# Performance work log

Measured on AMD Instinct MI355X. Metric: run time of the kernel, lower is better.

Reference implementation:

```python
import jax, jax.numpy as jnp
import numpy as np

EPS = 1e-5
B, CIN, COUT, H, W = 32, 512, 512, 56, 56
K = 4            # kernel_num
A = 32           # attention_channel = max(int(512*0.0625), 16)


def setup_inputs() -> dict:
    key = jax.random.key(0)
    ks = jax.random.split(key, 16)
    s = lambda fan: 1.0 / np.sqrt(fan)
    return {
        "x": jax.random.normal(ks[0], (B, CIN, H, W), jnp.float32),
        # attention trunk: global-avgpool -> fc -> bn -> relu
        "fc_w": jax.random.normal(ks[1], (A, CIN), jnp.float32) * s(CIN),
        "abn_g": jnp.ones((A,), jnp.float32),
        "abn_b": jnp.zeros((A,), jnp.float32),
        "abn_m": jax.random.normal(ks[2], (A,), jnp.float32) * 0.1,
        "abn_v": jax.random.uniform(ks[3], (A,), jnp.float32, 0.5, 1.5),
        # channel / filter / kernel attention heads
        "ch_w": jax.random.normal(ks[4], (CIN, A), jnp.float32) * s(A),
        "ch_b": jnp.zeros((CIN,), jnp.float32),
        "fl_w": jax.random.normal(ks[5], (COUT, A), jnp.float32) * s(A),
        "fl_b": jnp.zeros((COUT,), jnp.float32),
        "kn_w": jax.random.normal(ks[6], (K, A), jnp.float32) * s(A),
        "kn_b": jnp.zeros((K,), jnp.float32),
        # base 1x1 conv weight bank [kernel_num, out, in] (1x1 spatial squeezed)
        "weight": jax.random.normal(ks[7], (K, COUT, CIN), jnp.float32) * s(CIN),
        # output BatchNorm2d (eval mode: running stats)
        "bn_g": jnp.ones((COUT,), jnp.float32),
        "bn_b": jnp.zeros((COUT,), jnp.float32),
        "bn_m": jax.random.normal(ks[8], (COUT,), jnp.float32) * 0.1,
        "bn_v": jax.random.uniform(ks[9], (COUT,), jnp.float32, 0.5, 1.5),
    }


def reference(x, fc_w, abn_g, abn_b, abn_m, abn_v,
              ch_w, ch_b, fl_w, fl_b, kn_w, kn_b,
              weight, bn_g, bn_b, bn_m, bn_v):
    # ---- omni-dimensional attention (kernel_size=1 => spatial attn skipped) ----
    pooled = jnp.mean(x, axis=(2, 3))                       # [B, Cin]
    h = pooled @ fc_w.T                                     # [B, A]
    h = (h - abn_m) * (abn_g / jnp.sqrt(abn_v + EPS)) + abn_b
    h = jax.nn.relu(h)
    ch_att = jax.nn.sigmoid(h @ ch_w.T + ch_b)              # [B, Cin]
    fl_att = jax.nn.sigmoid(h @ fl_w.T + fl_b)              # [B, Cout]
    kn_att = jax.nn.softmax(h @ kn_w.T + kn_b, axis=1)      # [B, K] (temperature=1)
    # ---- per-sample aggregated 1x1 kernel + grouped(batch) pointwise conv ----
    agg_w = jnp.einsum('bk,koc->boc', kn_att, weight)       # [B, Cout, Cin]
    xm = x * ch_att[:, :, None, None]                       # channel attention
    y = jnp.einsum('bchw,boc->bohw', xm, agg_w)             # batched 1x1 conv
    y = y * fl_att[:, :, None, None]                        # filter attention
    # ---- BatchNorm2d (inference) ----
    inv = bn_g / jnp.sqrt(bn_v + EPS)
    y = (y - bn_m[None, :, None, None]) * inv[None, :, None, None] + bn_b[None, :, None, None]
    return y
```

## Files before the change

### kernel.cpp

```cpp
#include <hip/hip_runtime.h>
#include <math.h>

#define BATCH 32
#define CIN   512
#define COUT  512
#define HW    3136
#define KNUM  4
#define ADIM  32
#define EPS   1e-5f

static constexpr size_t XT_OFF    = 0;
static constexpr size_t WF_OFF    = 102760448;
static constexpr size_t PART_OFF  = 119537664;
static constexpr size_t CH_OFF    = 122748928;
static constexpr size_t FLINV_OFF = 122814464;
static constexpr size_t KN_OFF    = 122880000;

typedef __attribute__((ext_vector_type(8))) short short8;
typedef __attribute__((ext_vector_type(4))) float float4v;

typedef const unsigned int __attribute__((address_space(1)))* gas_ptr;
typedef unsigned int __attribute__((address_space(3)))* lds_ptr;

#define WAITVM(N) asm volatile("s_waitcnt vmcnt(" #N ")" ::: "memory")
#define BARRIER() do { __builtin_amdgcn_s_barrier(); asm volatile("" ::: "memory"); } while (0)

__device__ __forceinline__ unsigned short f2bf(float f) {
  unsigned int u = __float_as_uint(f);
  u += 0x7FFFu + ((u >> 16) & 1u);
  return (unsigned short)(u >> 16);
}

__global__ __launch_bounds__(256) void transpose_pool(
    const float* __restrict__ x, unsigned short* __restrict__ xT,
    float* __restrict__ part) {
  __shared__ unsigned short T[64 * 128];
  const int pb = blockIdx.x * 64;
  const int cb = blockIdx.y * 128;
  const int b  = blockIdx.z;
  const int t  = threadIdx.x;
  const int pq = t & 15;
  const int ch = t >> 4;

  float s[4][2];
  #pragma unroll
  for (int it = 0; it < 4; ++it) {
    const int cp = it * 16 + ch;
    const int c  = cb + cp * 2;
    const float* xp = x + (size_t)(b * CIN + c) * HW + pb + pq * 4;
    float4 v0 = *(const float4*)(xp);
    float4 v1 = *(const float4*)(xp + HW);
    s[it][0] = v0.x + v0.y + v0.z + v0.w;
    s[it][1] = v1.x + v1.y + v1.z + v1.w;
    const int dbase = (((cp >> 2) ^ pq) & 15) * 4 + (cp & 3);
    const float* f0 = (const float*)&v0;
    const float* f1 = (const float*)&v1;
    #pragma unroll
    for (int j = 0; j < 4; ++j) {
      const int p = pq * 4 + j;
      unsigned int w = (unsigned int)f2bf(f0[j]) |
                       ((unsigned int)f2bf(f1[j]) << 16);
      *(unsigned int*)&T[p * 128 + dbase * 2] = w;
    }
  }
  #pragma unroll
  for (int it = 0; it < 4; ++it) {
    #pragma unroll
    for (int e = 0; e < 2; ++e) {
      float v = s[it][e];
      #pragma unroll
      for (int off = 8; off > 0; off >>= 1) v += __shfl_down(v, off, 16);
      if (pq == 0)
        part[((size_t)b * 49 + blockIdx.x) * 512 + cb + (it * 16 + ch) * 2 + e] = v;
    }
  }
  __syncthreads();
  const int cg = t & 15;
  const int rb = t >> 4;
  #pragma unroll
  for (int itr = 0; itr < 4; ++itr) {
    const int p = rb + itr * 16;
    const int key = (p >> 2) & 15;
    uint4 r = *(const uint4*)&T[p * 128 + ((cg ^ key) & 15) * 8];
    *(uint4*)(xT + (size_t)(b * HW + pb + p) * CIN + cb + cg * 8) = r;
  }
}

__global__ __launch_bounds__(256) void attn_all(
    const float* __restrict__ part, const float* __restrict__ fc_w,
    const float* __restrict__ abn_g, const float* __restrict__ abn_b,
    const float* __restrict__ abn_m, const float* __restrict__ abn_v,
    const float* __restrict__ kn_w, const float* __restrict__ kn_b,
    const float* __restrict__ ch_w, const float* __restrict__ ch_b,
    const float* __restrict__ fl_w, const float* __restrict__ fl_b,
    const float* __restrict__ bn_g, const float* __restrict__ bn_v,
    float* __restrict__ ch_out, float* __restrict__ flinv_out,
    float* __restrict__ kn_out) {
  __shared__ float pooledS[CIN];
  __shared__ float hs[ADIM];
  const int b = blockIdx.x, t = threadIdx.x;
  #pragma unroll
  for (int idx = t; idx < CIN; idx += 256) {
    float s = 0.f;
    for (int j = 0; j < 49; ++j) s += part[((size_t)b * 49 + j) * 512 + idx];
    pooledS[idx] = s;
  }
  __syncthreads();
  {
    const int a = t >> 3, pz = t & 7;
    const float* fr = fc_w + a * CIN + pz * 64;
    const float* pp = pooledS + pz * 64;
    float s = 0.f;
    #pragma unroll 8
    for (int c = 0; c < 64; ++c) s += pp[c] * fr[c];
    #pragma unroll
    for (int off = 4; off > 0; off >>= 1) s += __shfl_down(s, off, 8);
    if (pz == 0) {
      s *= (1.0f / (float)HW);
      float vv = (s - abn_m[a]) * (abn_g[a] * rsqrtf(abn_v[a] + EPS)) + abn_b[a];
      hs[a] = fmaxf(vv, 0.f);
    }
  }
  __syncthreads();
  if (t == 0) {
    float lg[KNUM]; float mx = -1e30f;
    for (int k = 0; k < KNUM; ++k) {
      float acc = kn_b[k];
      for (int aa = 0; aa < ADIM; ++aa) acc += hs[aa] * kn_w[k * ADIM + aa];
      lg[k] = acc; mx = fmaxf(mx, acc);
    }
    float ssum = 0.f;
    for (int k = 0; k < KNUM; ++k) { lg[k] = expf(lg[k] - mx); ssum += lg[k]; }
    for (int k = 0; k < KNUM; ++k) kn_out[b * KNUM + k] = lg[k] / ssum;
  }
  #pragma unroll
  for (int c = t; c < CIN; c += 256) {
    const float* wr = ch_w + c * ADIM;
    float acc = ch_b[c];
    #pragma unroll
    for (int aa = 0; aa < ADIM; ++aa) acc += hs[aa] * wr[aa];
    ch_out[b * CIN + c] = 1.f / (1.f + expf(-acc));
  }
  #pragma unroll
  for (int o = t; o < COUT; o += 256) {
    const float* wr = fl_w + o * ADIM;
    float acc = fl_b[o];
    #pragma unroll
    for (int aa = 0; aa < ADIM; ++aa) acc += hs[aa] * wr[aa];
    float sig = 1.f / (1.f + expf(-acc));
    flinv_out[b * COUT + o] = sig * (bn_g[o] * rsqrtf(bn_v[o] + EPS));
  }
}

__global__ __launch_bounds__(256) void build_wf(
    const float* __restrict__ weight, const float* __restrict__ kn,
    const float* __restrict__ ch, const float* __restrict__ flinv,
    unsigned short* __restrict__ Wf) {
  const int och = blockIdx.x, b = blockIdx.y, t = threadIdx.x;
  const int o0 = och * 16;
  const float k0 = kn[b * KNUM + 0], k1 = kn[b * KNUM + 1];
  const float k2 = kn[b * KNUM + 2], k3 = kn[b * KNUM + 3];
  #pragma unroll
  for (int i = 0; i < 8; ++i) {
    int cell = i * 1024 + t * 4;
    int ol = cell >> 9, c = cell & 511;
    int o = o0 + ol;
    float fi = flinv[b * COUT + o];
    const float* wp = weight + (size_t)o * CIN + c;
    float4 w0 = *(const float4*)(wp);
    float4 w1 = *(const float4*)(wp + 1 * CIN * COUT);
    float4 w2 = *(const float4*)(wp + 2 * CIN * COUT);
    float4 w3 = *(const float4*)(wp + 3 * CIN * COUT);
    float4 cv = *(const float4*)(ch + b * CIN + c);
    ushort4 r;
    r.x = f2bf((k0 * w0.x + k1 * w1.x + k2 * w2.x + k3 * w3.x) * cv.x * fi);
    r.y = f2bf((k0 * w0.y + k1 * w1.y + k2 * w2.y + k3 * w3.y) * cv.y * fi);
    r.z = f2bf((k0 * w0.z + k1 * w1.z + k2 * w2.z + k3 * w3.z) * cv.z * fi);
    r.w = f2bf((k0 * w0.w + k1 * w1.w + k2 * w2.w + k3 * w3.w) * cv.w * fi);
    *(ushort4*)(Wf + (size_t)(b * COUT + o) * CIN + c) = r;
  }
}

__global__ __launch_bounds__(512, 2) void gemm_kernel(
    const unsigned short* __restrict__ xT, const unsigned short* __restrict__ Wf,
    const float* __restrict__ bn_g, const float* __restrict__ bn_b,
    const float* __restrict__ bn_m, const float* __restrict__ bn_v,
    float* __restrict__ y) {
  extern __shared__ unsigned short L[];
  const int id = blockIdx.x;
  const int wg = (id & 7) * 104 + (id >> 3);
  const int ot = wg & 1;
  const int rem = wg >> 1;
  const int pt = rem % 13;
  const int b  = rem / 13;
  const int o0 = ot * 256, p0 = pt * 256;
  const int t = threadIdx.x;
  const int wave = t >> 6, lane = t & 63;
  const int wm = wave >> 2, wn = wave & 3;

  const unsigned short* Ab = Wf + (size_t)b * COUT * CIN;
  const unsigned short* Bb = xT + (size_t)b * HW * CIN;

  const int rr = lane >> 2;
  const int gp = (lane & 3) ^ ((lane >> 3) & 3);
  const unsigned short* aS[2];
  const unsigned short* bS[2];
  int dOff[2];
  #pragma unroll
  for (int q = 0; q < 2; ++q) {
    const int m = q * 8 + wave;
    dOff[q] = m * 512;
    aS[q] = Ab + (size_t)(o0 + m * 16 + rr) * CIN + gp * 8;
    int brow = p0 + m * 16 + rr;
    if (brow > HW - 1) brow = HW - 1;
    bS[q] = Bb + (size_t)brow * CIN + gp * 8;
  }

  float4v acc[8][4];
  #pragma unroll
  for (int i = 0; i < 8; ++i)
    #pragma unroll
    for (int j = 0; j < 4; ++j)
      #pragma unroll
      for (int r = 0; r < 4; ++r) acc[i][j][r] = 0.f;

  const int arow = lane & 15;
  const int kgrp = lane >> 4;
  const int sl = (kgrp ^ ((arow >> 1) & 3)) * 8;

  auto stage = [&](int tt) {
    const int bufb = (tt & 3) * 16384;
    const int co = tt * 32;
    #pragma unroll
    for (int q = 0; q < 2; ++q)
      __builtin_amdgcn_global_load_lds((gas_ptr)(const void*)(aS[q] + co),
          (lds_ptr)(void*)&L[bufb + dOff[q]], 16, 0, 0);
    #pragma unroll
    for (int q = 0; q < 2; ++q)
      __builtin_amdgcn_global_load_lds((gas_ptr)(const void*)(bS[q] + co),
          (lds_ptr)(void*)&L[bufb + 8192 + dOff[q]], 16, 0, 0);
  };

  auto compute = [&](int tt) {
    const int bufb = (tt & 3) * 16384;
    short8 af[8], bv[4];
    #pragma unroll
    for (int i = 0; i < 8; ++i)
      af[i] = *(const short8*)&L[bufb + (wm * 128 + i * 16 + arow) * 32 + sl];
    #pragma unroll
    for (int j = 0; j < 4; ++j)
      bv[j] = *(const short8*)&L[bufb + 8192 + (wn * 64 + j * 16 + arow) * 32 + sl];
    __builtin_amdgcn_s_setprio(1);
    #pragma unroll
    for (int i = 0; i < 8; ++i)
      #pragma unroll
      for (int j = 0; j < 4; ++j)
        acc[i][j] = __builtin_amdgcn_mfma_f32_16x16x32_bf16(af[i], bv[j], acc[i][j], 0, 0, 0);
    __builtin_amdgcn_s_setprio(0);
  };

  stage(0); stage(1); stage(2);
  WAITVM(8);
  BARRIER();
  #pragma unroll 1
  for (int tt = 0; tt < 13; ++tt) {
    stage(tt + 3);
    compute(tt);
    WAITVM(8);
    BARRIER();
  }
  compute(13); WAITVM(4); BARRIER();
  compute(14); WAITVM(0); BARRIER();
  compute(15);

  const int rowq = (lane >> 4) * 4;
  const int coln = lane & 15;
  #pragma unroll
  for (int i = 0; i < 8; ++i) {
    const int obase = o0 + wm * 128 + i * 16 + rowq;
    float bet[4];
    #pragma unroll
    for (int r = 0; r < 4; ++r) {
      const int o = obase + r;
      const float inv = bn_g[o] * rsqrtf(bn_v[o] + EPS);
      bet[r] = bn_b[o] - bn_m[o] * inv;
    }
    #pragma unroll
    for (int j = 0; j < 4; ++j) {
      const int p = p0 + wn * 64 + j * 16 + coln;
      if (p < HW) {
        #pragma unroll
        for (int r = 0; r < 4; ++r)
          y[(size_t)(b * COUT + obase + r) * HW + p] = acc[i][j][r] + bet[r];
      }
    }
  }
}

extern "C" void kernel_launch(void* const* d_in, const int* in_sizes, int n_in,
                              void* d_out, int out_size, void* d_ws, size_t ws_size,
                              hipStream_t stream) {
  (void)in_sizes; (void)n_in; (void)out_size; (void)ws_size;
  const float* x     = (const float*)d_in[0];
  const float* fc_w  = (const float*)d_in[1];
  const float* abn_g = (const float*)d_in[2];
  const float* abn_b = (const float*)d_in[3];
  const float* abn_m = (const float*)d_in[4];
  const float* abn_v = (const float*)d_in[5];
  const float* ch_w  = (const float*)d_in[6];
  const float* ch_b  = (const float*)d_in[7];
  const float* fl_w  = (const float*)d_in[8];
  const float* fl_b  = (const float*)d_in[9];
  const float* kn_w  = (const float*)d_in[10];
  const float* kn_b  = (const float*)d_in[11];
  const float* weight= (const float*)d_in[12];
  const float* bn_g  = (const float*)d_in[13];
  const float* bn_b  = (const float*)d_in[14];
  const float* bn_m  = (const float*)d_in[15];
  const float* bn_v  = (const float*)d_in[16];
  float* out = (float*)d_out;

  char* ws = (char*)d_ws;
  unsigned short* xT = (unsigned short*)(ws + XT_OFF);
  unsigned short* Wf = (unsigned short*)(ws + WF_OFF);
  float* part  = (float*)(ws + PART_OFF);
  float* ch    = (float*)(ws + CH_OFF);
  float* flinv = (float*)(ws + FLINV_OFF);
  float* kn    = (float*)(ws + KN_OFF);

  static bool attr_done = false;
  if (!attr_done) {
    hipFuncSetAttribute((const void*)gemm_kernel,
                        hipFuncAttributeMaxDynamicSharedMemorySize, 131072);
    attr_done = true;
  }

  transpose_pool<<<dim3(49, 4, BATCH), 256, 0, stream>>>(x, xT, part);
  attn_all<<<BATCH, 256, 0, stream>>>(part, fc_w, abn_g, abn_b, abn_m, abn_v,
                                      kn_w, kn_b, ch_w, ch_b, fl_w, fl_b,
                                      bn_g, bn_v, ch, flinv, kn);
  build_wf<<<dim3(32, BATCH), 256, 0, stream>>>(weight, kn, ch, flinv, Wf);
  gemm_kernel<<<dim3(832), dim3(512), 131072, stream>>>(xT, Wf, bn_g, bn_b, bn_m, bn_v, out);
}
```

Baseline: 485.4 us.

## Shrink GEMM tile to 128x128 with double-buffered 4-wave blocks

Replaces the 256x256-tile, 8-wave, 4-stage-pipelined GEMM with a 128x128 tile using 4 waves and a two-buffer LDS pipeline with static shared memory. The grid becomes a plain 3D launch without the XCD-aware block remapping, and the priority hints and dynamic-LDS attribute setup are removed. The intent is more resident blocks per CU and finer-grained scheduling. The cost is halved operand reuse per tile, a shallower prefetch depth and an extra barrier per k-step.

```diff
diff --git a/kernel.cpp b/kernel.cpp
--- a/kernel.cpp
+++ b/kernel.cpp
@@ -23,7 +23,7 @@
 typedef unsigned int __attribute__((address_space(3)))* lds_ptr;
 
 #define WAITVM(N) asm volatile("s_waitcnt vmcnt(" #N ")" ::: "memory")
-#define BARRIER() do { __builtin_amdgcn_s_barrier(); asm volatile("" ::: "memory"); } while (0)
+#define WAITLGKM0() asm volatile("s_waitcnt lgkmcnt(0)" ::: "memory")
 
 __device__ __forceinline__ unsigned short f2bf(float f) {
   unsigned int u = __float_as_uint(f);
@@ -181,22 +181,17 @@
   }
 }
 
-__global__ __launch_bounds__(512, 2) void gemm_kernel(
+__global__ __launch_bounds__(256, 4) void gemm_kernel(
     const unsigned short* __restrict__ xT, const unsigned short* __restrict__ Wf,
     const float* __restrict__ bn_g, const float* __restrict__ bn_b,
     const float* __restrict__ bn_m, const float* __restrict__ bn_v,
     float* __restrict__ y) {
-  extern __shared__ unsigned short L[];
-  const int id = blockIdx.x;
-  const int wg = (id & 7) * 104 + (id >> 3);
-  const int ot = wg & 1;
-  const int rem = wg >> 1;
-  const int pt = rem % 13;
-  const int b  = rem / 13;
-  const int o0 = ot * 256, p0 = pt * 256;
+  __shared__ unsigned short L[2 * 8192];
+  const int ot = blockIdx.x, pt = blockIdx.y, b = blockIdx.z;
+  const int o0 = ot * 128, p0 = pt * 128;
   const int t = threadIdx.x;
   const int wave = t >> 6, lane = t & 63;
-  const int wm = wave >> 2, wn = wave & 3;
+  const int wm = wave & 1, wn = wave >> 1;
 
   const unsigned short* Ab = Wf + (size_t)b * COUT * CIN;
   const unsigned short* Bb = xT + (size_t)b * HW * CIN;
@@ -208,7 +203,7 @@
   int dOff[2];
   #pragma unroll
   for (int q = 0; q < 2; ++q) {
-    const int m = q * 8 + wave;
+    const int m = q * 4 + wave;
     dOff[q] = m * 512;
     aS[q] = Ab + (size_t)(o0 + m * 16 + rr) * CIN + gp * 8;
     int brow = p0 + m * 16 + rr;
@@ -216,9 +211,9 @@
     bS[q] = Bb + (size_t)brow * CIN + gp * 8;
   }
 
-  float4v acc[8][4];
-  #pragma unroll
-  for (int i = 0; i < 8; ++i)
+  float4v acc[4][4];
+  #pragma unroll
+  for (int i = 0; i < 4; ++i)
     #pragma unroll
     for (int j = 0; j < 4; ++j)
       #pragma unroll
@@ -229,7 +224,7 @@
   const int sl = (kgrp ^ ((arow >> 1) & 3)) * 8;
 
   auto stage = [&](int tt) {
-    const int bufb = (tt & 3) * 16384;
+    const int bufb = (tt & 1) * 8192;
     const int co = tt * 32;
     #pragma unroll
     for (int q = 0; q < 2; ++q)
@@ -238,46 +233,44 @@
     #pragma unroll
     for (int q = 0; q < 2; ++q)
       __builtin_amdgcn_global_load_lds((gas_ptr)(const void*)(bS[q] + co),
-          (lds_ptr)(void*)&L[bufb + 8192 + dOff[q]], 16, 0, 0);
+          (lds_ptr)(void*)&L[bufb + 4096 + dOff[q]], 16, 0, 0);
   };
 
   auto compute = [&](int tt) {
-    const int bufb = (tt & 3) * 16384;
-    short8 af[8], bv[4];
-    #pragma unroll
-    for (int i = 0; i < 8; ++i)
-      af[i] = *(const short8*)&L[bufb + (wm * 128 + i * 16 + arow) * 32 + sl];
+    const int bufb = (tt & 1) * 8192;
+    short8 af[4], bv[4];
+    #pragma unroll
+    for (int i = 0; i < 4; ++i)
+      af[i] = *(const short8*)&L[bufb + (wm * 64 + i * 16 + arow) * 32 + sl];
     #pragma unroll
     for (int j = 0; j < 4; ++j)
-      bv[j] = *(const short8*)&L[bufb + 8192 + (wn * 64 + j * 16 + arow) * 32 + sl];
-    __builtin_amdgcn_s_setprio(1);
-    #pragma unroll
-    for (int i = 0; i < 8; ++i)
+      bv[j] = *(const short8*)&L[bufb + 4096 + (wn * 64 + j * 16 + arow) * 32 + sl];
+    #pragma unroll
+    for (int i = 0; i < 4; ++i)
       #pragma unroll
       for (int j = 0; j < 4; ++j)
         acc[i][j] = __builtin_amdgcn_mfma_f32_16x16x32_bf16(af[i], bv[j], acc[i][j], 0, 0, 0);
-    __builtin_amdgcn_s_setprio(0);
   };
 
-  stage(0); stage(1); stage(2);
-  WAITVM(8);
-  BARRIER();
+  stage(0);
   #pragma unroll 1
-  for (int tt = 0; tt < 13; ++tt) {
-    stage(tt + 3);
+  for (int tt = 0; tt < 15; ++tt) {
+    stage(tt + 1);
+    WAITVM(4);
+    __builtin_amdgcn_s_barrier();
     compute(tt);
-    WAITVM(8);
-    BARRIER();
-  }
-  compute(13); WAITVM(4); BARRIER();
-  compute(14); WAITVM(0); BARRIER();
+    WAITLGKM0();
+    __builtin_amdgcn_s_barrier();
+  }
+  WAITVM(0);
+  __builtin_amdgcn_s_barrier();
   compute(15);
 
   const int rowq = (lane >> 4) * 4;
   const int coln = lane & 15;
   #pragma unroll
-  for (int i = 0; i < 8; ++i) {
-    const int obase = o0 + wm * 128 + i * 16 + rowq;
+  for (int i = 0; i < 4; ++i) {
+    const int obase = o0 + wm * 64 + i * 16 + rowq;
     float bet[4];
     #pragma unroll
     for (int r = 0; r < 4; ++r) {
@@ -328,17 +321,10 @@
   float* flinv = (float*)(ws + FLINV_OFF);
   float* kn    = (float*)(ws + KN_OFF);
 
-  static bool attr_done = false;
-  if (!attr_done) {
-    hipFuncSetAttribute((const void*)gemm_kernel,
-                        hipFuncAttributeMaxDynamicSharedMemorySize, 131072);
-    attr_done = true;
-  }
-
   transpose_pool<<<dim3(49, 4, BATCH), 256, 0, stream>>>(x, xT, part);
   attn_all<<<BATCH, 256, 0, stream>>>(part, fc_w, abn_g, abn_b, abn_m, abn_v,
                                       kn_w, kn_b, ch_w, ch_b, fl_w, fl_b,
                                       bn_g, bn_v, ch, flinv, kn);
   build_wf<<<dim3(32, BATCH), 256, 0, stream>>>(weight, kn, ch, flinv, Wf);
-  gemm_kernel<<<dim3(832), dim3(512), 131072, stream>>>(xT, Wf, bn_g, bn_b, bn_m, bn_v, out);
-}
+  gemm_kernel<<<dim3(4, 25, BATCH), 256, 0, stream>>>(xT, Wf, bn_g, bn_b, bn_m, bn_v, out);
+}
```

Measured after the change: 494.5 us. About the same (+1.9%).

## Restructure GEMM main loop to double-buffered 64-wide K tiles with interleaved staging

Applied to the files above, without the earlier changes.

The bf16 GEMM main loop moves from a 4-stage ring of 32-wide K tiles to a 2-stage double buffer of 64-wide K tiles. Each iteration is split into four MFMA quadrants, and the next tile's A and B loads into LDS are issued between LDS fragment reads and MFMA groups, so each buffer half is refilled once it has been read. The LDS swizzle changes to an 8-way XOR for the wider rows, and the launch bound drops the minimum-two-blocks-per-CU hint. The aim is fewer barriers and more MFMA work per sync. The cost is shallower prefetch depth, which may expose global latency, and register pressure may change without the occupancy hint.

```diff
diff --git a/kernel.cpp b/kernel.cpp
--- a/kernel.cpp
+++ b/kernel.cpp
@@ -21,9 +21,6 @@
 
 typedef const unsigned int __attribute__((address_space(1)))* gas_ptr;
 typedef unsigned int __attribute__((address_space(3)))* lds_ptr;
-
-#define WAITVM(N) asm volatile("s_waitcnt vmcnt(" #N ")" ::: "memory")
-#define BARRIER() do { __builtin_amdgcn_s_barrier(); asm volatile("" ::: "memory"); } while (0)
 
 __device__ __forceinline__ unsigned short f2bf(float f) {
   unsigned int u = __float_as_uint(f);
@@ -181,7 +178,7 @@
   }
 }
 
-__global__ __launch_bounds__(512, 2) void gemm_kernel(
+__global__ __launch_bounds__(512) void gemm_kernel(
     const unsigned short* __restrict__ xT, const unsigned short* __restrict__ Wf,
     const float* __restrict__ bn_g, const float* __restrict__ bn_b,
     const float* __restrict__ bn_m, const float* __restrict__ bn_v,
@@ -201,20 +198,38 @@
   const unsigned short* Ab = Wf + (size_t)b * COUT * CIN;
   const unsigned short* Bb = xT + (size_t)b * HW * CIN;
 
-  const int rr = lane >> 2;
-  const int gp = (lane & 3) ^ ((lane >> 3) & 3);
-  const unsigned short* aS[2];
-  const unsigned short* bS[2];
-  int dOff[2];
-  #pragma unroll
-  for (int q = 0; q < 2; ++q) {
-    const int m = q * 8 + wave;
-    dOff[q] = m * 512;
-    aS[q] = Ab + (size_t)(o0 + m * 16 + rr) * CIN + gp * 8;
-    int brow = p0 + m * 16 + rr;
+  const int sr = lane >> 3;
+  const int gsrc = (lane & 7) ^ sr;
+  const unsigned short* aSrc[4];
+  const unsigned short* bSrc[4];
+  int aDst[4], bDst[4];
+  #pragma unroll
+  for (int q = 0; q < 4; ++q) {
+    const int rloc = q * 64 + wave * 8;
+    aDst[q] = rloc * 64;
+    bDst[q] = 16384 + rloc * 64;
+    aSrc[q] = Ab + (size_t)(o0 + rloc + sr) * CIN + gsrc * 8;
+    int brow = p0 + rloc + sr;
     if (brow > HW - 1) brow = HW - 1;
-    bS[q] = Bb + (size_t)brow * CIN + gp * 8;
-  }
+    bSrc[q] = Bb + (size_t)brow * CIN + gsrc * 8;
+  }
+
+  auto stageA = [&](int kt) {
+    const int bb = (kt & 1) * 32768;
+    const int co = kt * 64;
+    #pragma unroll
+    for (int q = 0; q < 4; ++q)
+      __builtin_amdgcn_global_load_lds((gas_ptr)(const void*)(aSrc[q] + co),
+          (lds_ptr)(void*)&L[bb + aDst[q]], 16, 0, 0);
+  };
+  auto stageB = [&](int kt) {
+    const int bb = (kt & 1) * 32768;
+    const int co = kt * 64;
+    #pragma unroll
+    for (int q = 0; q < 4; ++q)
+      __builtin_amdgcn_global_load_lds((gas_ptr)(const void*)(bSrc[q] + co),
+          (lds_ptr)(void*)&L[bb + bDst[q]], 16, 0, 0);
+  };
 
   float4v acc[8][4];
   #pragma unroll
@@ -226,52 +241,86 @@
 
   const int arow = lane & 15;
   const int kgrp = lane >> 4;
-  const int sl = (kgrp ^ ((arow >> 1) & 3)) * 8;
-
-  auto stage = [&](int tt) {
-    const int bufb = (tt & 3) * 16384;
-    const int co = tt * 32;
-    #pragma unroll
-    for (int q = 0; q < 2; ++q)
-      __builtin_amdgcn_global_load_lds((gas_ptr)(const void*)(aS[q] + co),
-          (lds_ptr)(void*)&L[bufb + dOff[q]], 16, 0, 0);
-    #pragma unroll
-    for (int q = 0; q < 2; ++q)
-      __builtin_amdgcn_global_load_lds((gas_ptr)(const void*)(bS[q] + co),
-          (lds_ptr)(void*)&L[bufb + 8192 + dOff[q]], 16, 0, 0);
-  };
-
-  auto compute = [&](int tt) {
-    const int bufb = (tt & 3) * 16384;
-    short8 af[8], bv[4];
-    #pragma unroll
-    for (int i = 0; i < 8; ++i)
-      af[i] = *(const short8*)&L[bufb + (wm * 128 + i * 16 + arow) * 32 + sl];
-    #pragma unroll
-    for (int j = 0; j < 4; ++j)
-      bv[j] = *(const short8*)&L[bufb + 8192 + (wn * 64 + j * 16 + arow) * 32 + sl];
+  const int sl0 = ((kgrp    ) ^ (arow & 7)) * 8;
+  const int sl1 = ((4 + kgrp) ^ (arow & 7)) * 8;
+
+  stageA(0); stageB(0);
+  __syncthreads();
+
+  #pragma unroll 1
+  for (int kt = 0; kt < 8; ++kt) {
+    const int ab  = (kt & 1) * 32768;
+    const int bb2 = ab + 16384;
+    short8 a0[4][2], a1[4][2], bv[4][2];
+
+    #pragma unroll
+    for (int il = 0; il < 4; ++il) {
+      const int r = (wm * 128 + il * 16 + arow) * 64;
+      a0[il][0] = *(const short8*)&L[ab + r + sl0];
+      a0[il][1] = *(const short8*)&L[ab + r + sl1];
+    }
+    #pragma unroll
+    for (int jl = 0; jl < 2; ++jl) {
+      const int r = (wn * 64 + jl * 16 + arow) * 64;
+      bv[jl][0] = *(const short8*)&L[bb2 + r + sl0];
+      bv[jl][1] = *(const short8*)&L[bb2 + r + sl1];
+    }
+    if (kt < 7) stageA(kt + 1);
     __builtin_amdgcn_s_setprio(1);
     #pragma unroll
-    for (int i = 0; i < 8; ++i)
-      #pragma unroll
-      for (int j = 0; j < 4; ++j)
-        acc[i][j] = __builtin_amdgcn_mfma_f32_16x16x32_bf16(af[i], bv[j], acc[i][j], 0, 0, 0);
+    for (int il = 0; il < 4; ++il)
+      #pragma unroll
+      for (int jl = 0; jl < 2; ++jl) {
+        acc[il][jl] = __builtin_amdgcn_mfma_f32_16x16x32_bf16(a0[il][0], bv[jl][0], acc[il][jl], 0, 0, 0);
+        acc[il][jl] = __builtin_amdgcn_mfma_f32_16x16x32_bf16(a0[il][1], bv[jl][1], acc[il][jl], 0, 0, 0);
+      }
     __builtin_amdgcn_s_setprio(0);
-  };
-
-  stage(0); stage(1); stage(2);
-  WAITVM(8);
-  BARRIER();
-  #pragma unroll 1
-  for (int tt = 0; tt < 13; ++tt) {
-    stage(tt + 3);
-    compute(tt);
-    WAITVM(8);
-    BARRIER();
-  }
-  compute(13); WAITVM(4); BARRIER();
-  compute(14); WAITVM(0); BARRIER();
-  compute(15);
+
+    #pragma unroll
+    for (int jl = 0; jl < 2; ++jl) {
+      const int r = (wn * 64 + (2 + jl) * 16 + arow) * 64;
+      bv[2 + jl][0] = *(const short8*)&L[bb2 + r + sl0];
+      bv[2 + jl][1] = *(const short8*)&L[bb2 + r + sl1];
+    }
+    if (kt < 7) stageB(kt + 1);
+    __builtin_amdgcn_s_setprio(1);
+    #pragma unroll
+    for (int il = 0; il < 4; ++il)
+      #pragma unroll
+      for (int jl = 0; jl < 2; ++jl) {
+        acc[il][2 + jl] = __builtin_amdgcn_mfma_f32_16x16x32_bf16(a0[il][0], bv[2 + jl][0], acc[il][2 + jl], 0, 0, 0);
+        acc[il][2 + jl] = __builtin_amdgcn_mfma_f32_16x16x32_bf16(a0[il][1], bv[2 + jl][1], acc[il][2 + jl], 0, 0, 0);
+      }
+    __builtin_amdgcn_s_setprio(0);
+
+    #pragma unroll
+    for (int il = 0; il < 4; ++il) {
+      const int r = (wm * 128 + 64 + il * 16 + arow) * 64;
+      a1[il][0] = *(const short8*)&L[ab + r + sl0];
+      a1[il][1] = *(const short8*)&L[ab + r + sl1];
+    }
+    __builtin_amdgcn_s_setprio(1);
+    #pragma unroll
+    for (int il = 0; il < 4; ++il)
+      #pragma unroll
+      for (int jl = 0; jl < 2; ++jl) {
+        acc[4 + il][2 + jl] = __builtin_amdgcn_mfma_f32_16x16x32_bf16(a1[il][0], bv[2 + jl][0], acc[4 + il][2 + jl], 0, 0, 0);
+        acc[4 + il][2 + jl] = __builtin_amdgcn_mfma_f32_16x16x32_bf16(a1[il][1], bv[2 + jl][1], acc[4 + il][2 + jl], 0, 0, 0);
+      }
+    __builtin_amdgcn_s_setprio(0);
+
+    __builtin_amdgcn_s_setprio(1);
+    #pragma unroll
+    for (int il = 0; il < 4; ++il)
+      #pragma unroll
+      for (int jl = 0; jl < 2; ++jl) {
+        acc[4 + il][jl] = __builtin_amdgcn_mfma_f32_16x16x32_bf16(a1[il][0], bv[jl][0], acc[4 + il][jl], 0, 0, 0);
+        acc[4 + il][jl] = __builtin_amdgcn_mfma_f32_16x16x32_bf16(a1[il][1], bv[jl][1], acc[4 + il][jl], 0, 0, 0);
+      }
+    __builtin_amdgcn_s_setprio(0);
+
+    if (kt < 7) __syncthreads();
+  }
 
   const int rowq = (lane >> 4) * 4;
   const int coln = lane & 15;
```

New measurement: 477.1 us. No clear change (-1.7%).
